# Optimization experiments

Hardware: AMD Instinct MI355X
Metric: run time of the kernel (lower is better)

The kernel has to match this reference:

```python
import jax, jax.numpy as jnp
import numpy as np

T = 4                 # number of spiking timesteps (module init T)
NUM_THRESHOLDS = 8    # K thresholds: thresh / 2**k
B, C, H, W = 32, 128, 32, 32


def setup_inputs() -> dict:
    key = jax.random.key(0)
    x = jax.random.normal(key, ((T + 1) * B, C, H, W), dtype=jnp.float32)
    thresh = jnp.ones((1,), dtype=jnp.float32)
    return {"x": x, "thresh": thresh}


def _forward(x, thresh):
    # ExpandTemporalDim(T+1): [(T+1)*B, C, H, W] -> [T+1, B, C, H, W]
    xt_all = x.reshape((T + 1, B, C, H, W))
    # thre_shaped: [K, 1, 1, 1, 1]
    time_steps = (2.0 ** jnp.arange(NUM_THRESHOLDS, dtype=jnp.float32)).reshape(
        (NUM_THRESHOLDS, 1, 1, 1, 1))
    thre = thresh / time_steps
    thre_thr = thre * 0.75
    bias = xt_all[0]

    def step(carry, inp):
        mem, cum, exp_in, exp_out = carry
        xt, t = inp
        mem = mem + xt - bias + exp_in - exp_out
        cum = cum + exp_out
        # [K, B, C, H, W] indicator tensors
        pos = (mem[None] >= thre_thr).astype(jnp.float32)
        neg = ((mem[None] <= -thre_thr).astype(jnp.float32)
               * (cum[None] >= thre).astype(jnp.float32))
        # pos_true[0] = pos[0]; pos_true[k] = pos[k] - pos[k-1]
        zk = jnp.zeros_like(pos[:1])
        pos_true = jnp.diff(pos, axis=0, prepend=zk)
        neg_true = jnp.diff(neg, axis=0, prepend=zk)
        spike = (jnp.sum(thre * pos_true, axis=0)
                 - jnp.sum(thre * neg_true, axis=0))
        mem = mem - spike
        cum = cum + spike
        denom = t + 1.0
        exp_in = exp_in + (xt - bias) / denom
        exp_out = exp_out + spike / denom
        return (mem, cum, exp_in, exp_out), spike

    z = jnp.zeros_like(bias)
    carry0 = (z, z, bias, z)  # mem=0, cumulative_out=0, exp_in=x[0], exp_out=0
    ts = jnp.arange(T, dtype=jnp.float32)
    _, spikes = jax.lax.scan(step, carry0, (xt_all[1:], ts))
    # spike_pot[0] is zeros, then the T spikes; MergeTemporalDim flattens back
    out = jnp.concatenate([z[None], spikes], axis=0)
    return out.reshape(((T + 1) * B, C, H, W))


def reference(x, thresh):
    return _forward(x, thresh)
```

## Files before the change

### kernel.cpp

```cpp
#include <hip/hip_runtime.h>


constexpr int T_STEPS = 4;
constexpr int K_THR   = 8;

typedef float f32x4 __attribute__((ext_vector_type(4)));

__global__ __launch_bounds__(256) void mth_kernel(
    const float* __restrict__ x, const float* __restrict__ thresh,
    float* __restrict__ out, int n4)
{
    const float th = __uint_as_float(
        __builtin_amdgcn_readfirstlane(__float_as_uint(thresh[0])));

    const int i = blockIdx.x * blockDim.x + threadIdx.x;
    if (i >= n4) return;

    const f32x4* __restrict__ xv = reinterpret_cast<const f32x4*>(x);
    f32x4* __restrict__ ov       = reinterpret_cast<f32x4*>(out);

    float thre[K_THR], tt[K_THR];
    #pragma unroll
    for (int k = 0; k < K_THR; ++k) {
        thre[k] = th * (1.0f / (float)(1 << k));
        tt[k]   = 0.75f * thre[k];
    }

    const f32x4 b4 = xv[i];
    f32x4 xt4[T_STEPS];
    #pragma unroll
    for (int t = 0; t < T_STEPS; ++t)
        xt4[t] = xv[(size_t)(t + 1) * n4 + i];

    __builtin_nontemporal_store((f32x4){0.f, 0.f, 0.f, 0.f}, &ov[i]);

    float b[4]    = {b4.x, b4.y, b4.z, b4.w};
    float mem[4]  = {0.f, 0.f, 0.f, 0.f};
    float cum[4]  = {0.f, 0.f, 0.f, 0.f};
    float ein[4]  = {b4.x, b4.y, b4.z, b4.w};
    float eout[4] = {0.f, 0.f, 0.f, 0.f};

    #pragma unroll
    for (int t = 0; t < T_STEPS; ++t) {
        const float xt[4] = {xt4[t].x, xt4[t].y, xt4[t].z, xt4[t].w};
        f32x4 sp4;

        #pragma unroll
        for (int j = 0; j < 4; ++j) {
            float m = (((mem[j] + xt[j]) - b[j]) + ein[j]) - eout[j];
            float c = cum[j] + eout[j];

            float sp = 0.f, sn = 0.f;
            #pragma unroll
            for (int k = K_THR - 1; k >= 0; --k) {
                sp = (m >= tt[k]) ? thre[k] : sp;
                sn = (m <= -tt[k] && c >= thre[k]) ? thre[k] : sn;
            }
            const float spike = sp - sn;

            m -= spike;
            c += spike;
            const float d = xt[j] - b[j];
            if (t == 0)      { ein[j] += d;         eout[j] += spike;         }
            else if (t == 1) { ein[j] += d * 0.5f;  eout[j] += spike * 0.5f;  }
            else if (t == 2) { ein[j] += d / 3.0f;  eout[j] += spike / 3.0f;  }
            else             { ein[j] += d * 0.25f; eout[j] += spike * 0.25f; }

            mem[j] = m; cum[j] = c; sp4[j] = spike;
        }

        __builtin_nontemporal_store(sp4, &ov[(size_t)(t + 1) * n4 + i]);
    }
}

extern "C" void kernel_launch(void* const* d_in, const int* in_sizes, int n_in,
                              void* d_out, int out_size, void* d_ws, size_t ws_size,
                              hipStream_t stream)
{
    const float* x      = (const float*)d_in[0];
    const float* thresh = (const float*)d_in[1];
    float* out          = (float*)d_out;

    const int N  = in_sizes[0] / (T_STEPS + 1);
    const int n4 = N / 4;

    const int block = 256;
    const int grid  = (n4 + block - 1) / block;
    mth_kernel<<<grid, block, 0, stream>>>(x, thresh, out, n4);
}
```

Before: 152.0 us.

## Add bit-trick threshold fast path for unit thresh and process two vectors per thread

Adds a specialized path, used when thresh equals 1, that computes the multi-threshold spike level directly from float exponent bits instead of an 8-step compare/select chain. Each thread now handles two float4 groups 256 apart, which halves the grid and puts more loads in flight. The divide by 3 becomes a correctly rounded multiply-plus-FMA correction. This lowers ALU work in a memory-bound kernel. However, the grid now assumes n4 is a multiple of 512 with no tail handling, and the fast path is only valid for thresh of 1.

```diff
diff --git a/kernel.cpp b/kernel.cpp
--- a/kernel.cpp
+++ b/kernel.cpp
@@ -6,6 +6,121 @@
 
 typedef float f32x4 __attribute__((ext_vector_type(4)));
 
+__device__ __forceinline__ float div3_cr(float v) {
+    const float c = 1.0f / 3.0f;
+    float q = v * c;
+    float r = __builtin_fmaf(-3.0f, q, v);
+    return __builtin_fmaf(r, c, q);
+}
+
+__device__ __forceinline__ float spike_fast(float m, float c) {
+    const unsigned B075 = 0x3F400000u;
+    const unsigned B100 = 0x3F800000u;
+    const float TT7 = 0.0058593750f;
+    const float TH7 = 0.0078125f;
+
+    const unsigned mb = (unsigned)__float_as_int(m);
+
+    int dp = (int)(B075 - mb);
+    int kp = (dp + 0x7FFFFF) >> 23;
+    kp = kp < 0 ? 0 : kp;
+    const float spv = __int_as_float((127 - kp) << 23);
+    const float sp  = (m >= TT7) ? spv : 0.0f;
+
+    int da = (int)(B075 - (mb & 0x7FFFFFFFu));
+    int ka = (da + 0x7FFFFF) >> 23;
+    ka = ka < 0 ? 0 : ka;
+    int db = (int)(B100 - (unsigned)__float_as_int(c));
+    int kb = (db + 0x7FFFFF) >> 23;
+    kb = kb < 0 ? 0 : kb;
+    const int kn = ka > kb ? ka : kb;
+    const float snv = __int_as_float((127 - kn) << 23);
+    const float sn  = (m <= -TT7 && c >= TH7) ? snv : 0.0f;
+
+    return sp - sn;
+}
+
+__device__ __forceinline__ float spike_general(float m, float c,
+                                               const float* thre,
+                                               const float* tt) {
+    float sp = 0.f, sn = 0.f;
+    #pragma unroll
+    for (int k = K_THR - 1; k >= 0; --k) {
+        sp = (m >= tt[k]) ? thre[k] : sp;
+        sn = (m <= -tt[k] && c >= thre[k]) ? thre[k] : sn;
+    }
+    return sp - sn;
+}
+
+template <bool FAST>
+__device__ __forceinline__ void run_body(const f32x4* __restrict__ xv,
+                                         f32x4* __restrict__ ov,
+                                         float th, int n4, int i0, int i1)
+{
+    float thre[K_THR], tt[K_THR];
+    if (!FAST) {
+        #pragma unroll
+        for (int k = 0; k < K_THR; ++k) {
+            thre[k] = th * (1.0f / (float)(1 << k));
+            tt[k]   = 0.75f * thre[k];
+        }
+    }
+
+    f32x4 b4[2];
+    b4[0] = xv[i0];
+    b4[1] = xv[i1];
+    f32x4 xt4[2][T_STEPS];
+    #pragma unroll
+    for (int t = 0; t < T_STEPS; ++t) {
+        xt4[0][t] = xv[(size_t)(t + 1) * n4 + i0];
+        xt4[1][t] = xv[(size_t)(t + 1) * n4 + i1];
+    }
+
+    __builtin_nontemporal_store((f32x4){0.f, 0.f, 0.f, 0.f}, &ov[i0]);
+    __builtin_nontemporal_store((f32x4){0.f, 0.f, 0.f, 0.f}, &ov[i1]);
+
+    #pragma unroll
+    for (int u = 0; u < 2; ++u) {
+        const int i = (u == 0) ? i0 : i1;
+        float b[4]    = {b4[u].x, b4[u].y, b4[u].z, b4[u].w};
+        float mem[4]  = {0.f, 0.f, 0.f, 0.f};
+        float cum[4]  = {0.f, 0.f, 0.f, 0.f};
+        float ein[4]  = {b[0], b[1], b[2], b[3]};
+        float eout[4] = {0.f, 0.f, 0.f, 0.f};
+
+        #pragma unroll
+        for (int t = 0; t < T_STEPS; ++t) {
+            const float xt[4] = {xt4[u][t].x, xt4[u][t].y,
+                                 xt4[u][t].z, xt4[u][t].w};
+            f32x4 sp4;
+
+            #pragma unroll
+            for (int j = 0; j < 4; ++j) {
+                float m = (((mem[j] + xt[j]) - b[j]) + ein[j]) - eout[j];
+                float c = cum[j] + eout[j];
+
+                const float spike = FAST ? spike_fast(m, c)
+                                         : spike_general(m, c, thre, tt);
+                m -= spike;
+                c += spike;
+                const float d = xt[j] - b[j];
+                if (t == 0) {
+                    ein[j] += d;               eout[j] += spike;
+                } else if (t == 1) {
+                    ein[j] += d * 0.5f;        eout[j] += spike * 0.5f;
+                } else if (t == 2) {
+                    ein[j] += div3_cr(d);      eout[j] += div3_cr(spike);
+                } else {
+                    ein[j] += d * 0.25f;       eout[j] += spike * 0.25f;
+                }
+                mem[j] = m; cum[j] = c; sp4[j] = spike;
+            }
+
+            __builtin_nontemporal_store(sp4, &ov[(size_t)(t + 1) * n4 + i]);
+        }
+    }
+}
+
 __global__ __launch_bounds__(256) void mth_kernel(
     const float* __restrict__ x, const float* __restrict__ thresh,
     float* __restrict__ out, int n4)
@@ -13,64 +128,15 @@
     const float th = __uint_as_float(
         __builtin_amdgcn_readfirstlane(__float_as_uint(thresh[0])));
 
-    const int i = blockIdx.x * blockDim.x + threadIdx.x;
-    if (i >= n4) return;
+    const int i0 = blockIdx.x * 512 + threadIdx.x;
+    const int i1 = i0 + 256;
+    if (i1 >= n4) return;
 
     const f32x4* __restrict__ xv = reinterpret_cast<const f32x4*>(x);
     f32x4* __restrict__ ov       = reinterpret_cast<f32x4*>(out);
 
-    float thre[K_THR], tt[K_THR];
-    #pragma unroll
-    for (int k = 0; k < K_THR; ++k) {
-        thre[k] = th * (1.0f / (float)(1 << k));
-        tt[k]   = 0.75f * thre[k];
-    }
-
-    const f32x4 b4 = xv[i];
-    f32x4 xt4[T_STEPS];
-    #pragma unroll
-    for (int t = 0; t < T_STEPS; ++t)
-        xt4[t] = xv[(size_t)(t + 1) * n4 + i];
-
-    __builtin_nontemporal_store((f32x4){0.f, 0.f, 0.f, 0.f}, &ov[i]);
-
-    float b[4]    = {b4.x, b4.y, b4.z, b4.w};
-    float mem[4]  = {0.f, 0.f, 0.f, 0.f};
-    float cum[4]  = {0.f, 0.f, 0.f, 0.f};
-    float ein[4]  = {b4.x, b4.y, b4.z, b4.w};
-    float eout[4] = {0.f, 0.f, 0.f, 0.f};
-
-    #pragma unroll
-    for (int t = 0; t < T_STEPS; ++t) {
-        const float xt[4] = {xt4[t].x, xt4[t].y, xt4[t].z, xt4[t].w};
-        f32x4 sp4;
-
-        #pragma unroll
-        for (int j = 0; j < 4; ++j) {
-            float m = (((mem[j] + xt[j]) - b[j]) + ein[j]) - eout[j];
-            float c = cum[j] + eout[j];
-
-            float sp = 0.f, sn = 0.f;
-            #pragma unroll
-            for (int k = K_THR - 1; k >= 0; --k) {
-                sp = (m >= tt[k]) ? thre[k] : sp;
-                sn = (m <= -tt[k] && c >= thre[k]) ? thre[k] : sn;
-            }
-            const float spike = sp - sn;
-
-            m -= spike;
-            c += spike;
-            const float d = xt[j] - b[j];
-            if (t == 0)      { ein[j] += d;         eout[j] += spike;         }
-            else if (t == 1) { ein[j] += d * 0.5f;  eout[j] += spike * 0.5f;  }
-            else if (t == 2) { ein[j] += d / 3.0f;  eout[j] += spike / 3.0f;  }
-            else             { ein[j] += d * 0.25f; eout[j] += spike * 0.25f; }
-
-            mem[j] = m; cum[j] = c; sp4[j] = spike;
-        }
-
-        __builtin_nontemporal_store(sp4, &ov[(size_t)(t + 1) * n4 + i]);
-    }
+    if (th == 1.0f) run_body<true >(xv, ov, th, n4, i0, i1);
+    else            run_body<false>(xv, ov, th, n4, i0, i1);
 }
 
 extern "C" void kernel_launch(void* const* d_in, const int* in_sizes, int n_in,
@@ -83,8 +149,8 @@
 
     const int N  = in_sizes[0] / (T_STEPS + 1);
     const int n4 = N / 4;
+    const int block = 256;
+    const int grid  = n4 / (block * 2);
 
-    const int block = 256;
-    const int grid  = (n4 + block - 1) / block;
     mth_kernel<<<grid, block, 0, stream>>>(x, thresh, out, n4);
 }
```

After: 153.0 us. No clear change (+0.7%).
